# Kernel tuning notes

Measured on AMD Instinct MI355X. Metric: run time of the kernel, lower is better.

Reference implementation:

```python
import jax, jax.numpy as jnp
import numpy as np

N_NODES = 100000
N_EDGES = 1600000
IN_DIM = 256
HIDDEN = 128
N_CLASSES = 40


def gcn_conv(x, W, b, src, dst, n_nodes):
    """torch_geometric GCNConv: transform -> add self-loops -> sym-normalized sum-aggregate -> +bias."""
    h = x @ W  # [N, out]
    loop = jnp.arange(n_nodes, dtype=src.dtype)
    src2 = jnp.concatenate([src, loop])
    dst2 = jnp.concatenate([dst, loop])
    # degree with self-loops (edge weight 1)
    deg = jax.ops.segment_sum(jnp.ones_like(dst2, dtype=h.dtype), dst2, num_segments=n_nodes)
    dinv = jnp.where(deg > 0, jax.lax.rsqrt(deg), 0.0)
    norm = dinv[src2] * dinv[dst2]  # [E+N]
    msg = h[src2] * norm[:, None]   # [E+N, out] gather + scale
    out = jax.ops.segment_sum(msg, dst2, num_segments=n_nodes)
    return out + b


def setup_inputs() -> dict:
    key = jax.random.key(0)
    k1, k2, k3, k4 = jax.random.split(key, 4)
    x = jax.random.normal(k1, (N_NODES, IN_DIM), dtype=jnp.float32)
    edge_index = jax.random.randint(k2, (2, N_EDGES), 0, N_NODES, dtype=jnp.int64)
    W1 = jax.random.normal(k3, (IN_DIM, HIDDEN), dtype=jnp.float32) * (1.0 / np.sqrt(IN_DIM))
    b1 = jnp.zeros((HIDDEN,), dtype=jnp.float32)
    W2 = jax.random.normal(k4, (HIDDEN, N_CLASSES), dtype=jnp.float32) * (1.0 / np.sqrt(HIDDEN))
    b2 = jnp.zeros((N_CLASSES,), dtype=jnp.float32)
    return {"x": x, "edge_index": edge_index, "W1": W1, "b1": b1, "W2": W2, "b2": b2}


def reference(x, edge_index, W1, b1, W2, b2):
    src, dst = edge_index[0], edge_index[1]
    h = gcn_conv(x, W1, b1, src, dst, N_NODES)
    h = jax.nn.relu(h)
    # dropout p=0.5 is identity in eval mode
    out = gcn_conv(h, W2, b2, src, dst, N_NODES)
    return out
```

## Files before the change

### kernel.cpp

```cpp
#include <hip/hip_runtime.h>
#include <hip/hip_bf16.h>
#include <hip/hip_fp16.h>

#define N_NODES 100000
#define N_EDGES 1600000
#define IN_DIM 256
#define HIDDEN 128
#define NCLS 40
#define NCLS_PAD 48

#define N_BUCKETS 256
#define NPB 391
#define BCAP 8192
#define EPT 8
#define BIN_WG 2048
#define BIN_BLOCKS 782
#define GEMM1_BLOCKS 782

typedef __attribute__((ext_vector_type(8))) _Float16 half8;
typedef __attribute__((ext_vector_type(4))) _Float16 half4f;
typedef __attribute__((ext_vector_type(4))) float floatx4;


__global__ __launch_bounds__(256) void k_prep(const float* __restrict__ W1, __half* __restrict__ W1T,
                                              const float* __restrict__ W2, __half* __restrict__ W2T,
                                              int* __restrict__ bfill) {
    const int t = threadIdx.x;
    if (blockIdx.x < 128) {
        int i = blockIdx.x * 256 + t;
        int k = i >> 7, n = i & 127;
        W1T[n * IN_DIM + k] = __float2half_rn(W1[i]);
    } else if (blockIdx.x == 128) {
        for (int i = t; i < NCLS_PAD * HIDDEN; i += 256) {
            int n = i >> 7, k = i & 127;
            W2T[n * HIDDEN + k] = (n < NCLS) ? __float2half_rn(W2[k * NCLS + n]) : __float2half_rn(0.f);
        }
    } else {
        bfill[t] = 0;
    }
}


__global__ __launch_bounds__(256, 4) void k_binmm(const int* __restrict__ src, const int* __restrict__ dst,
                                                  int* __restrict__ bfill,
                                                  unsigned long long* __restrict__ bpair,
                                                  const float* __restrict__ X,
                                                  const __half* __restrict__ W1T,
                                                  __half* __restrict__ H1s) {
    __shared__ __align__(16) char smraw[21504];
    const int t = threadIdx.x;
    const int half_id = blockIdx.x >> 1;

    if ((blockIdx.x & 1) == 0) {
        int* hist   = (int*)smraw;
        int* bstart = hist + 256;
        int* gbase  = bstart + 256;
        unsigned long long* stage = (unsigned long long*)(smraw + 3072);
        unsigned char* bid = (unsigned char*)(smraw + 3072 + 16384);
        hist[t] = 0;
        __syncthreads();
        const long e0 = (long)half_id * BIN_WG;
        const int n_valid = (int)min((long)BIN_WG, (long)N_EDGES - e0);
        int msrc[EPT], mdst[EPT], moff[EPT];
        #pragma unroll
        for (int i = 0; i < EPT; i++) {
            long e = e0 + t + i * 256;
            if (e < N_EDGES) {
                msrc[i] = src[e];
                mdst[i] = dst[e];
                moff[i] = atomicAdd(&hist[mdst[i] / NPB], 1);
            } else {
                mdst[i] = -1;
            }
        }
        __syncthreads();
        if (t < 64) {
            int carry = 0;
            #pragma unroll
            for (int c = 0; c < 4; c++) {
                int idx = c * 64 + t;
                int hv = hist[idx];
                int s = hv;
                #pragma unroll
                for (int d2 = 1; d2 < 64; d2 <<= 1) {
                    int u = __shfl_up(s, d2, 64);
                    if (t >= d2) s += u;
                }
                bstart[idx] = carry + (s - hv);
                carry += __shfl(s, 63, 64);
            }
        }
        __syncthreads();
        int h = hist[t];
        gbase[t] = (h > 0) ? atomicAdd(&bfill[t], h) : 0;
        #pragma unroll
        for (int i = 0; i < EPT; i++) {
            if (mdst[i] >= 0) {
                int b = mdst[i] / NPB;
                int pos = bstart[b] + moff[i];
                stage[pos] = ((unsigned long long)(unsigned)mdst[i] << 32) | (unsigned)msrc[i];
                bid[pos] = (unsigned char)b;
            }
        }
        __syncthreads();
        for (int i = t; i < n_valid; i += 256) {
            int b = bid[i];
            int dest = gbase[b] + (i - bstart[b]);
            bpair[(long)b * BCAP + dest] = stage[i];
        }
        return;
    }

    const int wave = t >> 6;
    const int lane = t & 63;
    const int m16  = lane & 15;
    const int kq   = lane >> 4;
    const int row0 = half_id * 128;
    const int arow0 = row0 + wave * 32 + m16;
    const int arow1 = arow0 + 16;
    const bool va0 = arow0 < N_NODES;
    const bool va1 = arow1 < N_NODES;
    const float* pX0 = X + (long)arow0 * IN_DIM + kq * 8;
    const float* pX1 = X + (long)arow1 * IN_DIM + kq * 8;
    const __half* pB0 = W1T + m16 * IN_DIM + kq * 8;
    const float4 z4 = make_float4(0.f, 0.f, 0.f, 0.f);

    floatx4 acc[2][8];
    #pragma unroll
    for (int mt = 0; mt < 2; mt++)
        #pragma unroll
        for (int i = 0; i < 8; i++) acc[mt][i] = (floatx4)0.f;

    float4 curA[2][2], nxtA[2][2];
    if (va0) { curA[0][0] = *(const float4*)pX0; curA[0][1] = *(const float4*)(pX0 + 4); }
    else     { curA[0][0] = z4; curA[0][1] = z4; }
    if (va1) { curA[1][0] = *(const float4*)pX1; curA[1][1] = *(const float4*)(pX1 + 4); }
    else     { curA[1][0] = z4; curA[1][1] = z4; }

    #pragma unroll
    for (int s = 0; s < 8; s++) {
        if (s < 7) {
            const float* q0 = pX0 + (s + 1) * 32;
            const float* q1 = pX1 + (s + 1) * 32;
            if (va0) { nxtA[0][0] = *(const float4*)q0; nxtA[0][1] = *(const float4*)(q0 + 4); }
            else     { nxtA[0][0] = z4; nxtA[0][1] = z4; }
            if (va1) { nxtA[1][0] = *(const float4*)q1; nxtA[1][1] = *(const float4*)(q1 + 4); }
            else     { nxtA[1][0] = z4; nxtA[1][1] = z4; }
        }
        half8 a0, a1;
        a0[0] = (_Float16)curA[0][0].x; a0[1] = (_Float16)curA[0][0].y;
        a0[2] = (_Float16)curA[0][0].z; a0[3] = (_Float16)curA[0][0].w;
        a0[4] = (_Float16)curA[0][1].x; a0[5] = (_Float16)curA[0][1].y;
        a0[6] = (_Float16)curA[0][1].z; a0[7] = (_Float16)curA[0][1].w;
        a1[0] = (_Float16)curA[1][0].x; a1[1] = (_Float16)curA[1][0].y;
        a1[2] = (_Float16)curA[1][0].z; a1[3] = (_Float16)curA[1][0].w;
        a1[4] = (_Float16)curA[1][1].x; a1[5] = (_Float16)curA[1][1].y;
        a1[6] = (_Float16)curA[1][1].z; a1[7] = (_Float16)curA[1][1].w;
        const __half* pB = pB0 + s * 32;
        #pragma unroll
        for (int nt = 0; nt < 8; nt++) {
            half8 b = *(const half8*)(pB + nt * 16 * IN_DIM);
            acc[0][nt] = __builtin_amdgcn_mfma_f32_16x16x32_f16(a0, b, acc[0][nt], 0, 0, 0);
            acc[1][nt] = __builtin_amdgcn_mfma_f32_16x16x32_f16(a1, b, acc[1][nt], 0, 0, 0);
        }
        #pragma unroll
        for (int p = 0; p < 2; p++) {
            curA[p][0] = nxtA[p][0];
            curA[p][1] = nxtA[p][1];
        }
    }

    #pragma unroll
    for (int mt = 0; mt < 2; mt++) {
        const int gr0 = row0 + wave * 32 + mt * 16 + kq * 4;
        #pragma unroll
        for (int nt = 0; nt < 8; nt++) {
            int c = nt * 16 + m16;
            #pragma unroll
            for (int r = 0; r < 4; r++) {
                if (gr0 + r < N_NODES)
                    H1s[(long)(gr0 + r) * HIDDEN + c] = __float2half_rn(acc[mt][nt][r]);
            }
        }
    }
}


__global__ __launch_bounds__(256) void k_build(const int* __restrict__ bfill,
                                               const unsigned long long* __restrict__ bpair,
                                               int* __restrict__ row_ptr, float* __restrict__ dinv,
                                               int* __restrict__ col) {
    __shared__ int h[NPB];
    __shared__ int pfx[NPB];
    __shared__ int sred[4];
    const int b  = blockIdx.x;
    const int nb = b * NPB;
    const int nn = min(NPB, N_NODES - nb);
    const int t  = threadIdx.x;
    int v = (t < b) ? bfill[t] : 0;
    #pragma unroll
    for (int dl = 32; dl > 0; dl >>= 1) v += __shfl_down(v, dl, 64);
    if ((t & 63) == 0) sred[t >> 6] = v;
    for (int i = t; i < NPB; i += 256) h[i] = 0;
    __syncthreads();
    const int base_b = sred[0] + sred[1] + sred[2] + sred[3];
    const int n = bfill[b];
    for (int i = t; i < n; i += 256) {
        int dd = (int)(bpair[(long)b * BCAP + i] >> 32);
        atomicAdd(&h[dd - nb], 1);
    }
    __syncthreads();
    if (t < 64) {
        int carry = 0;
        #pragma unroll
        for (int c = 0; c < (NPB + 63) / 64; c++) {
            int idx = c * 64 + t;
            int hv = (idx < nn) ? h[idx] : 0;
            int s = hv;
            #pragma unroll
            for (int d2 = 1; d2 < 64; d2 <<= 1) {
                int u = __shfl_up(s, d2, 64);
                if (t >= d2) s += u;
            }
            if (idx < nn) {
                int ex = base_b + carry + (s - hv);
                pfx[idx] = ex;
                row_ptr[nb + idx] = ex;
                dinv[nb + idx] = rsqrtf((float)(hv + 1));
            }
            carry += __shfl(s, 63, 64);
        }
    }
    __syncthreads();
    for (int i = t; i < nn; i += 256) h[i] = 0;
    __syncthreads();
    for (int i = t; i < n; i += 256) {
        unsigned long long p = bpair[(long)b * BCAP + i];
        int dd = (int)(p >> 32);
        int ss = (int)(p & 0xFFFFFFFFu);
        int pos = pfx[dd - nb] + atomicAdd(&h[dd - nb], 1);
        col[pos] = ss;
    }
    if (b == 0 && t == 0) row_ptr[N_NODES] = N_EDGES;
}


__global__ __launch_bounds__(256) void k_agg1g2(const __half* __restrict__ H1s,
                                                const int* __restrict__ row_ptr,
                                                const int* __restrict__ col,
                                                const float* __restrict__ dinv,
                                                const float* __restrict__ b1,
                                                const __half* __restrict__ W2T,
                                                __half* __restrict__ H2s) {
    __shared__ __align__(16) _Float16 rows[16][136];
    const int wave = threadIdx.x >> 6;
    const int lane = threadIdx.x & 63;
    const __half2* base = (const __half2*)H1s;
    const float2 bb = ((const float2*)b1)[lane];
    const int d00 = blockIdx.x * 16 + wave * 4;

    #pragma unroll
    for (int i = 0; i < 4; i++) {
        const int d = d00 + i;
        const int e0 = __builtin_amdgcn_readfirstlane(row_ptr[d]);
        const int e1 = __builtin_amdgcn_readfirstlane(row_ptr[d + 1]);
        const float dd = dinv[d];
        float ax = 0.f, ay = 0.f;
        int e = e0;
        for (; e + 7 < e1; e += 8) {
            int s0 = col[e],     s1 = col[e + 1], s2 = col[e + 2], s3 = col[e + 3];
            int s4 = col[e + 4], s5 = col[e + 5], s6 = col[e + 6], s7 = col[e + 7];
            float d0 = dinv[s0], d1 = dinv[s1], d2 = dinv[s2], d3 = dinv[s3];
            float d4 = dinv[s4], d5 = dinv[s5], d6 = dinv[s6], d7 = dinv[s7];
            float2 f0 = __half22float2(base[(long)s0 * 64 + lane]);
            float2 f1 = __half22float2(base[(long)s1 * 64 + lane]);
            float2 f2 = __half22float2(base[(long)s2 * 64 + lane]);
            float2 f3 = __half22float2(base[(long)s3 * 64 + lane]);
            float2 f4 = __half22float2(base[(long)s4 * 64 + lane]);
            float2 f5 = __half22float2(base[(long)s5 * 64 + lane]);
            float2 f6 = __half22float2(base[(long)s6 * 64 + lane]);
            float2 f7 = __half22float2(base[(long)s7 * 64 + lane]);
            ax += d0 * f0.x + d1 * f1.x + d2 * f2.x + d3 * f3.x
                + d4 * f4.x + d5 * f5.x + d6 * f6.x + d7 * f7.x;
            ay += d0 * f0.y + d1 * f1.y + d2 * f2.y + d3 * f3.y
                + d4 * f4.y + d5 * f5.y + d6 * f6.y + d7 * f7.y;
        }
        for (; e + 3 < e1; e += 4) {
            int s0 = col[e], s1 = col[e + 1], s2 = col[e + 2], s3 = col[e + 3];
            float d0 = dinv[s0], d1 = dinv[s1], d2 = dinv[s2], d3 = dinv[s3];
            float2 f0 = __half22float2(base[(long)s0 * 64 + lane]);
            float2 f1 = __half22float2(base[(long)s1 * 64 + lane]);
            float2 f2 = __half22float2(base[(long)s2 * 64 + lane]);
            float2 f3 = __half22float2(base[(long)s3 * 64 + lane]);
            ax += d0 * f0.x + d1 * f1.x + d2 * f2.x + d3 * f3.x;
            ay += d0 * f0.y + d1 * f1.y + d2 * f2.y + d3 * f3.y;
        }
        for (; e < e1; e++) {
            int s = col[e];
            float dv = dinv[s];
            float2 f = __half22float2(base[(long)s * 64 + lane]);
            ax += dv * f.x; ay += dv * f.y;
        }
        float2 fs = __half22float2(base[(long)d * 64 + lane]);
        ax += dd * fs.x; ay += dd * fs.y;
        float ox = fmaxf(dd * ax + bb.x, 0.f) * dd;
        float oy = fmaxf(dd * ay + bb.y, 0.f) * dd;
        *(__half2*)&rows[wave * 4 + i][lane * 2] =
            __halves2half2(__float2half_rn(ox), __float2half_rn(oy));
    }
    __syncthreads();

    if (wave < 3) {
        const int m16 = lane & 15;
        const int kq  = lane >> 4;
        floatx4 acc = (floatx4)0.f;
        #pragma unroll
        for (int ks = 0; ks < 4; ks++) {
            half8 a = *(const half8*)&rows[m16][ks * 32 + kq * 8];
            half8 b = *(const half8*)&W2T[(wave * 16 + m16) * HIDDEN + ks * 32 + kq * 8];
            acc = __builtin_amdgcn_mfma_f32_16x16x32_f16(a, b, acc, 0, 0, 0);
        }
        const int c = wave * 16 + m16;
        if (c < NCLS) {
            const int gr0 = blockIdx.x * 16 + kq * 4;
            #pragma unroll
            for (int r = 0; r < 4; r++)
                H2s[(long)(gr0 + r) * NCLS + c] = __float2half_rn(acc[r]);
        }
    }
}


__global__ __launch_bounds__(256) void k_agg2(const __half* __restrict__ H2s,
                                              const int* __restrict__ row_ptr,
                                              const int* __restrict__ col,
                                              const float* __restrict__ dinv,
                                              const float* __restrict__ b2,
                                              float* __restrict__ out) {
    const int wave = threadIdx.x >> 6;
    const int lane = threadIdx.x & 63;
    const int g = lane / 10;
    const int f = lane - g * 10;
    const int d = blockIdx.x * 24 + wave * 6 + g;
    const bool act = (g < 6) && (d < N_NODES);
    int e0 = 0, e1 = 0;
    if (act) { e0 = row_ptr[d]; e1 = row_ptr[d + 1]; }
    const half4f* base4 = (const half4f*)H2s;
    float s0 = 0.f, s1 = 0.f, s2 = 0.f, s3 = 0.f;
    int e = e0;
    while (__any(e < e1)) {
        #pragma unroll
        for (int u = 0; u < 4; u++) {
            if (e + u < e1) {
                half4f v = base4[(long)col[e + u] * 10 + f];
                s0 += (float)v[0]; s1 += (float)v[1]; s2 += (float)v[2]; s3 += (float)v[3];
            }
        }
        e += 4;
    }
    if (act) {
        half4f v = base4[(long)d * 10 + f];
        s0 += (float)v[0]; s1 += (float)v[1]; s2 += (float)v[2]; s3 += (float)v[3];
        float dd = dinv[d];
        float4 bbv = ((const float4*)b2)[f];
        float4 o = make_float4(dd * s0 + bbv.x, dd * s1 + bbv.y, dd * s2 + bbv.z, dd * s3 + bbv.w);
        ((float4*)out)[(long)d * 10 + f] = o;
    }
}


extern "C" void kernel_launch(void* const* d_in, const int* in_sizes, int n_in,
                              void* d_out, int out_size, void* d_ws, size_t ws_size,
                              hipStream_t stream) {
    const float* x  = (const float*)d_in[0];
    const int*   ei = (const int*)d_in[1];
    const float* W1 = (const float*)d_in[2];
    const float* b1 = (const float*)d_in[3];
    const float* W2 = (const float*)d_in[4];
    const float* b2 = (const float*)d_in[5];
    const int* srcE = ei;
    const int* dstE = ei + N_EDGES;

    int*   row_ptr = (int*)d_ws;
    int*   bfill   = row_ptr + 100032;
    int*   col     = bfill + 256;
    float* dinv    = (float*)(col + N_EDGES);
    __half* H1s    = (__half*)(dinv + 100032);
    __half* H2s    = H1s + (long)N_NODES * HIDDEN;
    __half* W1T    = H2s + (long)N_NODES * NCLS;
    __half* W2T    = W1T + IN_DIM * HIDDEN;
    unsigned long long* bpair = (unsigned long long*)(W2T + NCLS_PAD * HIDDEN);

    k_prep   <<<130, 256, 0, stream>>>(W1, W1T, W2, W2T, bfill);
    k_binmm  <<<BIN_BLOCKS + GEMM1_BLOCKS, 256, 0, stream>>>(srcE, dstE, bfill, bpair, x, W1T, H1s);
    k_build  <<<N_BUCKETS, 256, 0, stream>>>(bfill, bpair, row_ptr, dinv, col);
    k_agg1g2 <<<N_NODES / 16, 256, 0, stream>>>(H1s, row_ptr, col, dinv, b1, W2T, H2s);
    k_agg2   <<<(N_NODES + 23) / 24, 256, 0, stream>>>(H2s, row_ptr, col, dinv, b2, (float*)d_out);
}
```

Before: 369.1 us.

## Stage W1 in LDS for GEMM, enlarge binning chunks, unroll aggregation deeper

The fused bin+GEMM kernel now gives the first 391 blocks the binning work, each handling 4096 edges (EPT 16), and the remaining blocks the GEMM, instead of interleaving even/odd blocks. In the GEMM, W1T is copied into padded LDS in two 128-wide K halves, replacing per-wave global loads of B. The layer-2 aggregation loop is unrolled 8 instead of 4. The larger LDS footprint and the dropped occupancy hint may lower occupancy, and the extra syncthreads in the GEMM add stalls.

Result: faster. 334.2 us (-9.5%).

```diff
diff --git a/kernel.cpp b/kernel.cpp
--- a/kernel.cpp
+++ b/kernel.cpp
@@ -12,9 +12,9 @@
 #define N_BUCKETS 256
 #define NPB 391
 #define BCAP 8192
-#define EPT 8
-#define BIN_WG 2048
-#define BIN_BLOCKS 782
+#define EPT 16
+#define BIN_WG 4096
+#define BIN_BLOCKS 391
 #define GEMM1_BLOCKS 782
 
 typedef __attribute__((ext_vector_type(8))) _Float16 half8;
@@ -41,25 +41,24 @@
 }
 
 
-__global__ __launch_bounds__(256, 4) void k_binmm(const int* __restrict__ src, const int* __restrict__ dst,
-                                                  int* __restrict__ bfill,
-                                                  unsigned long long* __restrict__ bpair,
-                                                  const float* __restrict__ X,
-                                                  const __half* __restrict__ W1T,
-                                                  __half* __restrict__ H1s) {
-    __shared__ __align__(16) char smraw[21504];
+__global__ __launch_bounds__(256) void k_binmm(const int* __restrict__ src, const int* __restrict__ dst,
+                                               int* __restrict__ bfill,
+                                               unsigned long long* __restrict__ bpair,
+                                               const float* __restrict__ X,
+                                               const __half* __restrict__ W1T,
+                                               __half* __restrict__ H1s) {
+    __shared__ __align__(16) char smraw[39936];
     const int t = threadIdx.x;
-    const int half_id = blockIdx.x >> 1;
-
-    if ((blockIdx.x & 1) == 0) {
+
+    if (blockIdx.x < BIN_BLOCKS) {
         int* hist   = (int*)smraw;
         int* bstart = hist + 256;
         int* gbase  = bstart + 256;
         unsigned long long* stage = (unsigned long long*)(smraw + 3072);
-        unsigned char* bid = (unsigned char*)(smraw + 3072 + 16384);
+        unsigned char* bid = (unsigned char*)(smraw + 3072 + 32768);
         hist[t] = 0;
         __syncthreads();
-        const long e0 = (long)half_id * BIN_WG;
+        const long e0 = (long)blockIdx.x * BIN_WG;
         const int n_valid = (int)min((long)BIN_WG, (long)N_EDGES - e0);
         int msrc[EPT], mdst[EPT], moff[EPT];
         #pragma unroll
@@ -111,18 +110,18 @@
         return;
     }
 
+    _Float16 (*Bsm)[136] = (_Float16(*)[136])smraw;
     const int wave = t >> 6;
     const int lane = t & 63;
     const int m16  = lane & 15;
     const int kq   = lane >> 4;
-    const int row0 = half_id * 128;
+    const int row0 = (blockIdx.x - BIN_BLOCKS) * 128;
     const int arow0 = row0 + wave * 32 + m16;
     const int arow1 = arow0 + 16;
     const bool va0 = arow0 < N_NODES;
     const bool va1 = arow1 < N_NODES;
     const float* pX0 = X + (long)arow0 * IN_DIM + kq * 8;
     const float* pX1 = X + (long)arow1 * IN_DIM + kq * 8;
-    const __half* pB0 = W1T + m16 * IN_DIM + kq * 8;
     const float4 z4 = make_float4(0.f, 0.f, 0.f, 0.f);
 
     floatx4 acc[2][8];
@@ -132,42 +131,50 @@
         for (int i = 0; i < 8; i++) acc[mt][i] = (floatx4)0.f;
 
     float4 curA[2][2], nxtA[2][2];
-    if (va0) { curA[0][0] = *(const float4*)pX0; curA[0][1] = *(const float4*)(pX0 + 4); }
-    else     { curA[0][0] = z4; curA[0][1] = z4; }
-    if (va1) { curA[1][0] = *(const float4*)pX1; curA[1][1] = *(const float4*)(pX1 + 4); }
-    else     { curA[1][0] = z4; curA[1][1] = z4; }
+    auto loadA2 = [&](float4 (*A)[2], int kbase) {
+        if (va0) { A[0][0] = *(const float4*)(pX0 + kbase); A[0][1] = *(const float4*)(pX0 + kbase + 4); }
+        else     { A[0][0] = z4; A[0][1] = z4; }
+        if (va1) { A[1][0] = *(const float4*)(pX1 + kbase); A[1][1] = *(const float4*)(pX1 + kbase + 4); }
+        else     { A[1][0] = z4; A[1][1] = z4; }
+    };
+
+    loadA2(curA, 0);
 
     #pragma unroll
-    for (int s = 0; s < 8; s++) {
-        if (s < 7) {
-            const float* q0 = pX0 + (s + 1) * 32;
-            const float* q1 = pX1 + (s + 1) * 32;
-            if (va0) { nxtA[0][0] = *(const float4*)q0; nxtA[0][1] = *(const float4*)(q0 + 4); }
-            else     { nxtA[0][0] = z4; nxtA[0][1] = z4; }
-            if (va1) { nxtA[1][0] = *(const float4*)q1; nxtA[1][1] = *(const float4*)(q1 + 4); }
-            else     { nxtA[1][0] = z4; nxtA[1][1] = z4; }
-        }
-        half8 a0, a1;
-        a0[0] = (_Float16)curA[0][0].x; a0[1] = (_Float16)curA[0][0].y;
-        a0[2] = (_Float16)curA[0][0].z; a0[3] = (_Float16)curA[0][0].w;
-        a0[4] = (_Float16)curA[0][1].x; a0[5] = (_Float16)curA[0][1].y;
-        a0[6] = (_Float16)curA[0][1].z; a0[7] = (_Float16)curA[0][1].w;
-        a1[0] = (_Float16)curA[1][0].x; a1[1] = (_Float16)curA[1][0].y;
-        a1[2] = (_Float16)curA[1][0].z; a1[3] = (_Float16)curA[1][0].w;
-        a1[4] = (_Float16)curA[1][1].x; a1[5] = (_Float16)curA[1][1].y;
-        a1[6] = (_Float16)curA[1][1].z; a1[7] = (_Float16)curA[1][1].w;
-        const __half* pB = pB0 + s * 32;
-        #pragma unroll
-        for (int nt = 0; nt < 8; nt++) {
-            half8 b = *(const half8*)(pB + nt * 16 * IN_DIM);
-            acc[0][nt] = __builtin_amdgcn_mfma_f32_16x16x32_f16(a0, b, acc[0][nt], 0, 0, 0);
-            acc[1][nt] = __builtin_amdgcn_mfma_f32_16x16x32_f16(a1, b, acc[1][nt], 0, 0, 0);
-        }
-        #pragma unroll
-        for (int p = 0; p < 2; p++) {
-            curA[p][0] = nxtA[p][0];
-            curA[p][1] = nxtA[p][1];
-        }
+    for (int h = 0; h < 2; h++) {
+        #pragma unroll
+        for (int i = 0; i < 8; i++) {
+            int c = t + i * 256;
+            int n = c >> 4, k8 = c & 15;
+            *(half8*)&Bsm[n][k8 * 8] = *(const half8*)&W1T[n * IN_DIM + h * 128 + k8 * 8];
+        }
+        __syncthreads();
+        #pragma unroll
+        for (int s = 0; s < 4; s++) {
+            if (!(h == 1 && s == 3)) {
+                int kn = (s < 3) ? (h * 128 + (s + 1) * 32) : 128;
+                loadA2(nxtA, kn);
+            }
+            half8 a0, a1;
+            a0[0] = (_Float16)curA[0][0].x; a0[1] = (_Float16)curA[0][0].y;
+            a0[2] = (_Float16)curA[0][0].z; a0[3] = (_Float16)curA[0][0].w;
+            a0[4] = (_Float16)curA[0][1].x; a0[5] = (_Float16)curA[0][1].y;
+            a0[6] = (_Float16)curA[0][1].z; a0[7] = (_Float16)curA[0][1].w;
+            a1[0] = (_Float16)curA[1][0].x; a1[1] = (_Float16)curA[1][0].y;
+            a1[2] = (_Float16)curA[1][0].z; a1[3] = (_Float16)curA[1][0].w;
+            a1[4] = (_Float16)curA[1][1].x; a1[5] = (_Float16)curA[1][1].y;
+            a1[6] = (_Float16)curA[1][1].z; a1[7] = (_Float16)curA[1][1].w;
+            const _Float16* bbase = &Bsm[m16][s * 32 + kq * 8];
+            #pragma unroll
+            for (int nt = 0; nt < 8; nt++) {
+                half8 b = *(const half8*)(bbase + nt * 16 * 136);
+                acc[0][nt] = __builtin_amdgcn_mfma_f32_16x16x32_f16(a0, b, acc[0][nt], 0, 0, 0);
+                acc[1][nt] = __builtin_amdgcn_mfma_f32_16x16x32_f16(a1, b, acc[1][nt], 0, 0, 0);
+            }
+            #pragma unroll
+            for (int p = 0; p < 2; p++) { curA[p][0] = nxtA[p][0]; curA[p][1] = nxtA[p][1]; }
+        }
+        if (h == 0) __syncthreads();
     }
 
     #pragma unroll
@@ -350,13 +357,13 @@
     int e = e0;
     while (__any(e < e1)) {
         #pragma unroll
-        for (int u = 0; u < 4; u++) {
+        for (int u = 0; u < 8; u++) {
             if (e + u < e1) {
                 half4f v = base4[(long)col[e + u] * 10 + f];
                 s0 += (float)v[0]; s1 += (float)v[1]; s2 += (float)v[2]; s3 += (float)v[3];
             }
         }
-        e += 4;
+        e += 8;
     }
     if (act) {
         half4f v = base4[(long)d * 10 + f];
```
